# Kernel tuning notes

Hardware: AMD Instinct MI355X
Metric: run time of the kernel (lower is better)

Reference implementation:

```python
import jax, jax.numpy as jnp
from jax import lax
import numpy as np

B = 32          # batch
E = 768         # embedding_dim == hidden_dim (required for the module to run)
V = 8192        # vocabulary_size
MAX_LEN = 256   # max_seq_length


def setup_inputs() -> dict:
    key = jax.random.key(0)
    ks = jax.random.split(key, 10)
    s = 0.02
    return {
        "latent": jax.random.normal(ks[0], (B, E), jnp.float32),
        "W_lat": jax.random.normal(ks[1], (E, E), jnp.float32) * s,
        "b_lat": jnp.zeros((E,), jnp.float32),
        "emb":   jax.random.normal(ks[2], (V, E), jnp.float32) * s,
        "W_ih":  jax.random.normal(ks[3], (3 * E, E), jnp.float32) * s,
        "W_hh":  jax.random.normal(ks[4], (3 * E, E), jnp.float32) * s,
        "b_ih":  jnp.zeros((3 * E,), jnp.float32),
        "b_hh":  jnp.zeros((3 * E,), jnp.float32),
        "W_out": jax.random.normal(ks[5], (V, E), jnp.float32) * s,
        "b_out": jnp.zeros((V,), jnp.float32),
    }


def reference(latent, W_lat, b_lat, emb, W_ih, W_hh, b_ih, b_hh, W_out, b_out):
    # initial hidden state: projected latent, shape [B, E]
    h0 = latent @ W_lat.T + b_lat
    # decoder starts from token id 1 (<sos>)
    tok0 = jnp.ones((latent.shape[0],), jnp.int32)

    def step(carry, _):
        h, tok = carry
        x = emb[tok]                                  # [B, E] embedding lookup
        gi = x @ W_ih.T + b_ih                        # [B, 3E]
        gh = h @ W_hh.T + b_hh                        # [B, 3E]
        i_r, i_z, i_n = jnp.split(gi, 3, axis=-1)
        h_r, h_z, h_n = jnp.split(gh, 3, axis=-1)
        r = jax.nn.sigmoid(i_r + h_r)
        z = jax.nn.sigmoid(i_z + h_z)
        n = jnp.tanh(i_n + r * h_n)
        h_new = (1.0 - z) * n + z * h                 # torch GRU cell update
        pred = h_new @ W_out.T + b_out                # [B, V]
        tok_new = jnp.argmax(pred, axis=-1).astype(jnp.int32)  # greedy decode
        return (h_new, tok_new), pred

    _, preds = lax.scan(step, (h0, tok0), None, length=MAX_LEN)  # [T, B, V]
    return preds.transpose(1, 0, 2)                               # [B, T, V]
```

## Files before the change

### kernel.cpp

```cpp
#include <hip/hip_runtime.h>
#include <stdint.h>


typedef unsigned long long u64;
typedef unsigned int u32;
typedef _Float16 f16;
using half8 = __attribute__((ext_vector_type(8))) _Float16;
using f32x4 = __attribute__((ext_vector_type(4))) float;
using uint4v = __attribute__((ext_vector_type(4))) unsigned int;

#define E_ 768
#define V_ 8192
#define T_ 256
#define HP 24576
#define IH_PLANE (2304*768)
#define OUT_PLANE (8192*768)
#define NBLK 256

#define AGENT_LD(p)    __hip_atomic_load((p), __ATOMIC_RELAXED, __HIP_MEMORY_SCOPE_AGENT)
#define AGENT_ST(p,v)  __hip_atomic_store((p), (v), __ATOMIC_RELAXED, __HIP_MEMORY_SCOPE_AGENT)
#define AGENT_ADD(p,v) __hip_atomic_fetch_add((p), (v), __ATOMIC_RELAXED, __HIP_MEMORY_SCOPE_AGENT)

__device__ __forceinline__ f32x4 mfma16(half8 a, half8 b, f32x4 c){
  return __builtin_amdgcn_mfma_f32_16x16x32_f16(a, b, c, 0, 0, 0);
}
__device__ __forceinline__ void split2(float f, f16& hi, f16& lo){
  f16 h = (f16)f; hi = h; lo = (f16)((f - (float)h) * 4096.0f);
}
__device__ __forceinline__ u32 packh(float f){
  f16 h, l; split2(f, h, l);
  return (u32)__builtin_bit_cast(unsigned short, h) |
         ((u32)__builtin_bit_cast(unsigned short, l) << 16);
}
__device__ __forceinline__ float unpackh(u32 u){
  f16 h = __builtin_bit_cast(f16, (unsigned short)(u & 0xffffu));
  f16 l = __builtin_bit_cast(f16, (unsigned short)(u >> 16));
  return (float)h + (float)l * (1.0f/4096.0f);
}
__device__ __forceinline__ u64 packkey(float f, int v){
  u32 fb = __float_as_uint(f);
  u32 s  = fb ^ ((u32)((int32_t)fb>>31) | 0x80000000u);
  return ((u64)s<<32) | (u64)(0xFFFFFFFFu - (u32)v);
}

#define NB_CONV 1200
#define NB_H0   96
#define NG_IH   221184
#define NG_ALL  1228800

__global__ __launch_bounds__(256) void prep_k(
    const float* __restrict__ W_ih, const float* __restrict__ W_hh, const float* __restrict__ W_out,
    const float* __restrict__ latent, const float* __restrict__ W_lat, const float* __restrict__ b_lat,
    f16* __restrict__ Wih_s, f16* __restrict__ Whh_s, f16* __restrict__ Wout_s,
    float* __restrict__ h_f32, u32* __restrict__ h_seq, unsigned* __restrict__ bar)
{
  int blk = blockIdx.x;
  if (blk < NB_CONV){
    for (int g = blk*256 + threadIdx.x; g < NG_ALL; g += NB_CONV*256){
      const float* src; f16* hi; f16* lo; int off;
      if (g < NG_IH)        { src=W_ih; hi=Wih_s; lo=Wih_s+IH_PLANE; off=g*8; }
      else if (g < 2*NG_IH) { src=W_hh; hi=Whh_s; lo=Whh_s+IH_PLANE; off=(g-NG_IH)*8; }
      else                  { src=W_out; hi=Wout_s; lo=Wout_s+OUT_PLANE; off=(g-2*NG_IH)*8; }
      float4 a = *(const float4*)(src+off);
      float4 b = *(const float4*)(src+off+4);
      float fs[8] = {a.x,a.y,a.z,a.w,b.x,b.y,b.z,b.w};
      half8 vh, vl;
      #pragma unroll
      for (int j=0;j<8;j++){ f16 h,l; split2(fs[j],h,l); vh[j]=h; vl[j]=l; }
      *(half8*)(hi+off) = vh;
      *(half8*)(lo+off) = vl;
    }
  } else {
    if (blk==NB_CONV) bar[threadIdx.x] = 0;
    int tid = (blk-NB_CONV)*256 + threadIdx.x;
    int b = tid/768, e = tid - b*768;
    const float4* wr = (const float4*)(W_lat + (size_t)e*768);
    const float4* xr = (const float4*)(latent + (size_t)b*768);
    float s0=0.f,s1=0.f,s2=0.f,s3=0.f;
    for (int k=0;k<192;k++){
      float4 w = wr[k]; float4 x = xr[k];
      s0 += w.x*x.x; s1 += w.y*x.y; s2 += w.z*x.z; s3 += w.w*x.w;
    }
    float acc = b_lat[e] + ((s0+s1)+(s2+s3));
    h_f32[b*768+e] = acc;
    h_seq[b*768+e] = packh(acc);
  }
}

__global__ __launch_bounds__(512) void gitab_k(
    const float* __restrict__ emb, const f16* __restrict__ Wih_s, u32* __restrict__ gi_tab)
{
  __shared__ float red[3][8][2][64][4];
  const int bid = blockIdx.x, tid = threadIdx.x;
  const int tb = bid>>1, half = bid&1;
  const int w = tid>>6, lane = tid&63, col = lane&15, kg = lane>>4, kc = w;
  half8 ah[2][3], al[2][3];
  #pragma unroll
  for (int m=0;m<2;m++)
    #pragma unroll
    for (int i=0;i<3;i++){
      const float* src = emb + (size_t)(tb*32 + m*16 + col)*768 + kc*96 + i*32 + kg*8;
      float4 x0 = *(const float4*)src, x1 = *(const float4*)(src+4);
      float fs[8] = {x0.x,x0.y,x0.z,x0.w,x1.x,x1.y,x1.z,x1.w};
      half8 vh, vl;
      #pragma unroll
      for (int j=0;j<8;j++){ f16 h,l; split2(fs[j],h,l); vh[j]=h; vl[j]=l; }
      ah[m][i]=vh; al[m][i]=vl;
    }
  for (int g=0; g<24; ++g){
    #pragma unroll
    for (int j=0;j<3;j++){
      const int nt = half*72 + g*3 + j;
      f32x4 a0[2], a1[2];
      #pragma unroll
      for (int m=0;m<2;m++){ a0[m]=f32x4{0,0,0,0}; a1[m]=f32x4{0,0,0,0}; }
      #pragma unroll
      for (int i=0;i<3;i++){
        size_t o = (size_t)(nt*16+col)*768 + kc*96 + i*32 + kg*8;
        half8 bh = *(const half8*)(Wih_s + o);
        half8 bl = *(const half8*)(Wih_s + IH_PLANE + o);
        #pragma unroll
        for (int m=0;m<2;m++){
          a0[m] = mfma16(ah[m][i], bh, a0[m]);
          a1[m] = mfma16(ah[m][i], bl, a1[m]);
          a1[m] = mfma16(al[m][i], bh, a1[m]);
        }
      }
      #pragma unroll
      for (int m=0;m<2;m++){
        f32x4 v;
        #pragma unroll
        for (int r=0;r<4;r++) v[r] = a0[m][r] + a1[m][r]*(1.0f/4096.0f);
        *(f32x4*)&red[j][w][m][lane][0] = v;
      }
    }
    __syncthreads();
    if (w < 6){
      const int j = w>>1, m = w&1;
      f32x4 s = {0,0,0,0};
      #pragma unroll
      for (int ww=0; ww<8; ww++) s += *(const f32x4*)&red[j][ww][m][lane][0];
      const int nt = half*72 + g*3 + j;
      const int tokr = tb*32 + m*16 + kg*4;
      #pragma unroll
      for (int r=0;r<4;r++)
        gi_tab[(size_t)(tokr+r)*2304 + nt*16 + col] = packh(s[r]);
    }
    __syncthreads();
  }
}

__device__ __forceinline__ void gridbar(unsigned* bar, unsigned target){
  __syncthreads();
  if (threadIdx.x == 0){
    const int g = blockIdx.x & 7;
    unsigned old = AGENT_ADD(&bar[g*16], 1u);
    if (old == 32u*target - 1u)
      AGENT_ADD(&bar[128], 1u);
    int spins = 0;
    while (AGENT_LD(&bar[128]) < 8u*target){
      __builtin_amdgcn_s_sleep(1);
      if ((++spins & 2047) == 0)
        AGENT_ADD(&bar[128], 0u);
    }
  }
  __syncthreads();
}

__global__ __launch_bounds__(512, 2) void decode_k(
    const f16* __restrict__ Wout_s, const f16* __restrict__ Whh_s, const u32* __restrict__ gi_tab,
    float* __restrict__ gh_buf, const float* __restrict__ h_f32, u32* __restrict__ h_seq,
    u64* __restrict__ candbufT, const float* __restrict__ b_ih, const float* __restrict__ b_hh,
    const float* __restrict__ b_out, float* __restrict__ out, unsigned* __restrict__ bar)
{
  __shared__ float red[3][8][2][64][4];
  __shared__ u64 amkey[32];
  const int bid = blockIdx.x, tid = threadIdx.x;
  const int w = tid>>6, lane = tid&63, col = lane&15, kg = lane>>4, kc = w;

  __builtin_amdgcn_fence(__ATOMIC_ACQUIRE, "agent");
  __syncthreads();

  const f16* srcH[3] = {Wout_s, Wout_s, (bid<144)? Whh_s : Wout_s};
  const f16* srcL[3] = {Wout_s+OUT_PLANE, Wout_s+OUT_PLANE,
                        (bid<144)? Whh_s+IH_PLANE : Wout_s+OUT_PLANE};
  const int  rowb[3] = {bid*16, 4096+bid*16, (bid<144)? bid*16 : 0};
  half8 bf_h[3][3], bf_l[3][3];
  #pragma unroll
  for (int s=0;s<3;s++)
    #pragma unroll
    for (int i=0;i<3;i++){
      size_t o = (size_t)(rowb[s]+col)*768 + kc*96 + i*32 + kg*8;
      bf_h[s][i] = *(const half8*)(srcH[s] + o);
      bf_l[s][i] = *(const half8*)(srcL[s] + o);
    }
  float bo_reg[2];
  bo_reg[0] = b_out[bid*16 + col];
  bo_reg[1] = b_out[4096 + bid*16 + col];

  int cb = 0, ce = 0; float hreg = 0.f;
  float bir=0,biz=0,bin_=0,bhr=0,bhz=0,bhn=0;
  if (bid < 48){
    int gid = bid*512 + tid;
    cb = gid/768; ce = gid - cb*768;
    hreg = h_f32[cb*768 + ce];
    bir=b_ih[ce]; biz=b_ih[768+ce]; bin_=b_ih[1536+ce];
    bhr=b_hh[ce]; bhz=b_hh[768+ce]; bhn=b_hh[1536+ce];
  }

  unsigned bt = 0;
  for (int t=0; t<=256; ++t){
    if (tid < 32) amkey[tid] = 0;
    const u32* hbase = h_seq + (size_t)t*HP;
    uint4v qa[2][3], qb[2][3];
    #pragma unroll
    for (int m=0;m<2;m++)
      #pragma unroll
      for (int i=0;i<3;i++){
        const uint4v* hp = (const uint4v*)(hbase + (m*16+col)*768 + kc*96 + i*32 + kg*8);
        qa[m][i] = hp[0];
        qb[m][i] = hp[1];
      }
    half8 ah[2][3], al[2][3];
    #pragma unroll
    for (int m=0;m<2;m++)
      #pragma unroll
      for (int i=0;i<3;i++){
        uint4v wh, wl;
        u32 d[8] = {qa[m][i][0],qa[m][i][1],qa[m][i][2],qa[m][i][3],
                    qb[m][i][0],qb[m][i][1],qb[m][i][2],qb[m][i][3]};
        #pragma unroll
        for (int j=0;j<4;j++){
          u32 w0 = d[2*j], w1 = d[2*j+1];
          wh[j] = (w0 & 0xffffu) | (w1 << 16);
          wl[j] = (w0 >> 16) | (w1 & 0xffff0000u);
        }
        ah[m][i] = __builtin_bit_cast(half8, wh);
        al[m][i] = __builtin_bit_cast(half8, wl);
      }
    #pragma unroll
    for (int s=0;s<3;s++){
      f32x4 a0[2], a1[2];
      #pragma unroll
      for (int m=0;m<2;m++){ a0[m]=f32x4{0,0,0,0}; a1[m]=f32x4{0,0,0,0}; }
      #pragma unroll
      for (int i=0;i<3;i++)
        #pragma unroll
        for (int m=0;m<2;m++){
          a0[m] = mfma16(ah[m][i], bf_h[s][i], a0[m]);
          a1[m] = mfma16(ah[m][i], bf_l[s][i], a1[m]);
          a1[m] = mfma16(al[m][i], bf_h[s][i], a1[m]);
        }
      #pragma unroll
      for (int m=0;m<2;m++){
        f32x4 v;
        #pragma unroll
        for (int r=0;r<4;r++) v[r] = a0[m][r] + a1[m][r]*(1.0f/4096.0f);
        *(f32x4*)&red[s][w][m][lane][0] = v;
      }
    }
    __syncthreads();
    float sv[2][4];
    bool have_out = false;
    if (w < 3){
      const int s = w;
      float vm[2][4];
      #pragma unroll
      for (int m=0;m<2;m++){
        f32x4 sum = {0,0,0,0};
        #pragma unroll
        for (int ww=0; ww<8; ww++) sum += *(const f32x4*)&red[s][ww][m][lane][0];
        #pragma unroll
        for (int r=0;r<4;r++) vm[m][r] = sum[r];
      }
      if (s < 2){
        if (t >= 1){
          have_out = true;
          const int v = s*4096 + bid*16 + col;
          const float bo = bo_reg[s];
          #pragma unroll
          for (int m=0;m<2;m++)
            #pragma unroll
            for (int r=0;r<4;r++){
              const int b = m*16 + kg*4 + r;
              const float p = vm[m][r] + bo;
              sv[m][r] = p;
              u64 key = packkey(p, v);
              #pragma unroll
              for (int off=1; off<16; off<<=1){
                u64 o = __shfl_xor((unsigned long long)key, off);
                if (o > key) key = o;
              }
              if (col == 0) atomicMax(&amkey[b], key);
            }
        }
      } else if (bid < 144){
        const int gr = bid*16 + col;
        #pragma unroll
        for (int m=0;m<2;m++)
          #pragma unroll
          for (int r=0;r<4;r++)
            AGENT_ST(&gh_buf[(m*16+kg*4+r)*2304 + gr], vm[m][r]);
      }
    }
    __syncthreads();
    if (t >= 1 && tid < 32) AGENT_ST(&candbufT[(size_t)tid*256 + bid], amkey[tid]);
    if (t == 256){
      if (have_out){
        const int v = w*4096 + bid*16 + col;
        #pragma unroll
        for (int m=0;m<2;m++)
          #pragma unroll
          for (int r=0;r<4;r++)
            out[(size_t)(m*16+kg*4+r)*((size_t)T_*V_) + (size_t)(t-1)*V_ + v] = sv[m][r];
      }
      break;
    }
    gridbar(bar, ++bt);
    if (bid >= 48){
      if (have_out){
        const int v = w*4096 + bid*16 + col;
        #pragma unroll
        for (int m=0;m<2;m++)
          #pragma unroll
          for (int r=0;r<4;r++)
            out[(size_t)(m*16+kg*4+r)*((size_t)T_*V_) + (size_t)(t-1)*V_ + v] = sv[m][r];
      }
    } else {
      int tok = 1;
      if (t > 0){
        u64 k = 0;
        #pragma unroll
        for (int j=0;j<4;j++){
          u64 c = AGENT_LD(&candbufT[(size_t)cb*256 + lane + 64*j]);
          if (c > k) k = c;
        }
        #pragma unroll
        for (int off=1; off<64; off<<=1){
          u64 o = __shfl_xor((unsigned long long)k, off);
          if (o > k) k = o;
        }
        tok = (int)(0xFFFFFFFFu - (unsigned)(k & 0xFFFFFFFFull));
      }
      const u32* gp = gi_tab + (size_t)tok*2304 + ce;
      const float gir = unpackh(gp[0])    + bir;
      const float giz = unpackh(gp[768])  + biz;
      const float gin = unpackh(gp[1536]) + bin_;
      float* hb = gh_buf + cb*2304 + ce;
      const float ghr = AGENT_LD(hb)        + bhr;
      const float ghz = AGENT_LD(hb + 768)  + bhz;
      const float ghn = AGENT_LD(hb + 1536) + bhn;
      const float rr = 1.0f/(1.0f+expf(-(gir+ghr)));
      const float zz = 1.0f/(1.0f+expf(-(giz+ghz)));
      const float nn = tanhf(gin + rr*ghn);
      hreg = (1.0f-zz)*nn + zz*hreg;
      AGENT_ST(&h_seq[(size_t)(t+1)*HP + cb*768 + ce], packh(hreg));
      if (have_out){
        const int v = w*4096 + bid*16 + col;
        #pragma unroll
        for (int m=0;m<2;m++)
          #pragma unroll
          for (int r=0;r<4;r++)
            out[(size_t)(m*16+kg*4+r)*((size_t)T_*V_) + (size_t)(t-1)*V_ + v] = sv[m][r];
      }
    }
    gridbar(bar, ++bt);
  }
}

extern "C" void kernel_launch(void* const* d_in, const int* in_sizes, int n_in,
                              void* d_out, int out_size, void* d_ws, size_t ws_size,
                              hipStream_t stream){
  const float* latent = (const float*)d_in[0];
  const float* W_lat  = (const float*)d_in[1];
  const float* b_lat  = (const float*)d_in[2];
  const float* emb    = (const float*)d_in[3];
  const float* W_ih   = (const float*)d_in[4];
  const float* W_hh   = (const float*)d_in[5];
  const float* b_ih   = (const float*)d_in[6];
  const float* b_hh   = (const float*)d_in[7];
  const float* W_out  = (const float*)d_in[8];
  const float* b_out  = (const float*)d_in[9];
  float* out = (float*)d_out;
  (void)in_sizes; (void)n_in; (void)out_size; (void)ws_size;

  char* ws = (char*)d_ws;
  size_t off = 0;
  auto carve = [&](size_t bytes)->char*{
    char* p = ws + off; off += (bytes + 255) & ~(size_t)255; return p;
  };
  f16*      Wih_s  = (f16*)     carve((size_t)2*IH_PLANE*2);
  f16*      Whh_s  = (f16*)     carve((size_t)2*IH_PLANE*2);
  f16*      Wout_s = (f16*)     carve((size_t)2*OUT_PLANE*2);
  u32*      gi_tab = (u32*)     carve((size_t)8192*2304*4);
  float*    gh_buf = (float*)   carve((size_t)32*2304*4);
  float*    h_f32  = (float*)   carve((size_t)HP*4);
  u32*      h_seq  = (u32*)     carve((size_t)257*HP*4);
  u64*      candbufT=(u64*)     carve((size_t)32*256*8);
  unsigned* bar    = (unsigned*)carve(2048);

  hipLaunchKernelGGL(prep_k, dim3(NB_CONV+NB_H0), dim3(256), 0, stream,
                     W_ih, W_hh, W_out, latent, W_lat, b_lat,
                     Wih_s, Whh_s, Wout_s, h_f32, h_seq, bar);
  hipLaunchKernelGGL(gitab_k, dim3(512), dim3(512), 0, stream, emb, Wih_s, gi_tab);

  void* kargs[] = {
    (void*)&Wout_s, (void*)&Whh_s, (void*)&gi_tab, (void*)&gh_buf, (void*)&h_f32,
    (void*)&h_seq, (void*)&candbufT, (void*)&b_ih, (void*)&b_hh, (void*)&b_out,
    (void*)&out, (void*)&bar
  };
  (void)hipLaunchCooperativeKernel((void*)decode_k, dim3(NBLK), dim3(512), kargs, 0, stream);
}
```

Baseline: 3.083 ms.

## Pre-split hidden-state layout, flat grid barrier, interleaved gh buffer, earlier output stores

Stores the hidden state as separate hi/lo f16 halves in MFMA-ready 8-element groups, so the per-step A-operand load becomes direct half8 reads with no repacking. The grid barrier becomes a single level of 16 counters polled by one wavefront with __all, replacing the two-level counter scheme. gh_buf is interleaved per (batch, element) so the three gate values sit next to each other, and they are loaded earlier together with the logit stores. The h_seq writes use inline-asm short stores with sc0 sc1 plus a vmcnt wait, which depends on hardware-specific cache semantics for visibility to other blocks.

```diff
diff --git a/kernel.cpp b/kernel.cpp
--- a/kernel.cpp
+++ b/kernel.cpp
@@ -4,10 +4,10 @@
 
 typedef unsigned long long u64;
 typedef unsigned int u32;
+typedef unsigned short ush;
 typedef _Float16 f16;
 using half8 = __attribute__((ext_vector_type(8))) _Float16;
 using f32x4 = __attribute__((ext_vector_type(4))) float;
-using uint4v = __attribute__((ext_vector_type(4))) unsigned int;
 
 #define E_ 768
 #define V_ 8192
@@ -16,6 +16,8 @@
 #define IH_PLANE (2304*768)
 #define OUT_PLANE (8192*768)
 #define NBLK 256
+#define HS_STEP 49152
+#define HS_ROW  1536
 
 #define AGENT_LD(p)    __hip_atomic_load((p), __ATOMIC_RELAXED, __HIP_MEMORY_SCOPE_AGENT)
 #define AGENT_ST(p,v)  __hip_atomic_store((p), (v), __ATOMIC_RELAXED, __HIP_MEMORY_SCOPE_AGENT)
@@ -29,12 +31,11 @@
 }
 __device__ __forceinline__ u32 packh(float f){
   f16 h, l; split2(f, h, l);
-  return (u32)__builtin_bit_cast(unsigned short, h) |
-         ((u32)__builtin_bit_cast(unsigned short, l) << 16);
+  return (u32)__builtin_bit_cast(ush, h) | ((u32)__builtin_bit_cast(ush, l) << 16);
 }
 __device__ __forceinline__ float unpackh(u32 u){
-  f16 h = __builtin_bit_cast(f16, (unsigned short)(u & 0xffffu));
-  f16 l = __builtin_bit_cast(f16, (unsigned short)(u >> 16));
+  f16 h = __builtin_bit_cast(f16, (ush)(u & 0xffffu));
+  f16 l = __builtin_bit_cast(f16, (ush)(u >> 16));
   return (float)h + (float)l * (1.0f/4096.0f);
 }
 __device__ __forceinline__ u64 packkey(float f, int v){
@@ -83,7 +84,10 @@
     }
     float acc = b_lat[e] + ((s0+s1)+(s2+s3));
     h_f32[b*768+e] = acc;
-    h_seq[b*768+e] = packh(acc);
+    f16 hh, ll; split2(acc, hh, ll);
+    ush* hw = (ush*)h_seq + b*HS_ROW + (e>>3)*16 + (e&7);
+    hw[0] = __builtin_bit_cast(ush, hh);
+    hw[8] = __builtin_bit_cast(ush, ll);
   }
 }
 
@@ -152,16 +156,14 @@
 
 __device__ __forceinline__ void gridbar(unsigned* bar, unsigned target){
   __syncthreads();
-  if (threadIdx.x == 0){
-    const int g = blockIdx.x & 7;
-    unsigned old = AGENT_ADD(&bar[g*16], 1u);
-    if (old == 32u*target - 1u)
-      AGENT_ADD(&bar[128], 1u);
-    int spins = 0;
-    while (AGENT_LD(&bar[128]) < 8u*target){
+  if (threadIdx.x < 64){
+    if (threadIdx.x == 0) AGENT_ADD(&bar[(blockIdx.x & 15)*16], 1u);
+    const u32 goal = 16u*target;
+    const int lane = threadIdx.x;
+    for(;;){
+      u32 v = (lane < 16) ? AGENT_LD(&bar[lane*16]) : goal;
+      if (__all(v >= goal)) break;
       __builtin_amdgcn_s_sleep(1);
-      if ((++spins & 2047) == 0)
-        AGENT_ADD(&bar[128], 0u);
     }
   }
   __syncthreads();
@@ -207,36 +209,21 @@
     bir=b_ih[ce]; biz=b_ih[768+ce]; bin_=b_ih[1536+ce];
     bhr=b_hh[ce]; bhz=b_hh[768+ce]; bhn=b_hh[1536+ce];
   }
+  const int gr2 = bid*16 + col;
+  const int gg2 = gr2/768, ge2 = gr2 - (gr2/768)*768;
 
   unsigned bt = 0;
   for (int t=0; t<=256; ++t){
     if (tid < 32) amkey[tid] = 0;
-    const u32* hbase = h_seq + (size_t)t*HP;
-    uint4v qa[2][3], qb[2][3];
-    #pragma unroll
-    for (int m=0;m<2;m++)
-      #pragma unroll
-      for (int i=0;i<3;i++){
-        const uint4v* hp = (const uint4v*)(hbase + (m*16+col)*768 + kc*96 + i*32 + kg*8);
-        qa[m][i] = hp[0];
-        qb[m][i] = hp[1];
-      }
+    const ush* h16 = (const ush*)h_seq + (size_t)t*HS_STEP;
     half8 ah[2][3], al[2][3];
     #pragma unroll
     for (int m=0;m<2;m++)
       #pragma unroll
       for (int i=0;i<3;i++){
-        uint4v wh, wl;
-        u32 d[8] = {qa[m][i][0],qa[m][i][1],qa[m][i][2],qa[m][i][3],
-                    qb[m][i][0],qb[m][i][1],qb[m][i][2],qb[m][i][3]};
-        #pragma unroll
-        for (int j=0;j<4;j++){
-          u32 w0 = d[2*j], w1 = d[2*j+1];
-          wh[j] = (w0 & 0xffffu) | (w1 << 16);
-          wl[j] = (w0 >> 16) | (w1 & 0xffff0000u);
-        }
-        ah[m][i] = __builtin_bit_cast(half8, wh);
-        al[m][i] = __builtin_bit_cast(half8, wl);
+        const ush* hp = h16 + (m*16+col)*HS_ROW + (kc*12+i*4+kg)*16;
+        ah[m][i] = *(const half8*)(hp);
+        al[m][i] = *(const half8*)(hp+8);
       }
     #pragma unroll
     for (int s=0;s<3;s++){
@@ -295,12 +282,11 @@
             }
         }
       } else if (bid < 144){
-        const int gr = bid*16 + col;
         #pragma unroll
         for (int m=0;m<2;m++)
           #pragma unroll
           for (int r=0;r<4;r++)
-            AGENT_ST(&gh_buf[(m*16+kg*4+r)*2304 + gr], vm[m][r]);
+            AGENT_ST(&gh_buf[((size_t)(m*16+kg*4+r)*768 + ge2)*4 + gg2], vm[m][r]);
       }
     }
     __syncthreads();
@@ -327,6 +313,18 @@
             out[(size_t)(m*16+kg*4+r)*((size_t)T_*V_) + (size_t)(t-1)*V_ + v] = sv[m][r];
       }
     } else {
+      const float* hb4 = gh_buf + ((size_t)cb*768 + ce)*4;
+      const float ghr0 = AGENT_LD(hb4 + 0);
+      const float ghz0 = AGENT_LD(hb4 + 1);
+      const float ghn0 = AGENT_LD(hb4 + 2);
+      if (have_out){
+        const int v = w*4096 + bid*16 + col;
+        #pragma unroll
+        for (int m=0;m<2;m++)
+          #pragma unroll
+          for (int r=0;r<4;r++)
+            out[(size_t)(m*16+kg*4+r)*((size_t)T_*V_) + (size_t)(t-1)*V_ + v] = sv[m][r];
+      }
       int tok = 1;
       if (t > 0){
         u64 k = 0;
@@ -346,23 +344,20 @@
       const float gir = unpackh(gp[0])    + bir;
       const float giz = unpackh(gp[768])  + biz;
       const float gin = unpackh(gp[1536]) + bin_;
-      float* hb = gh_buf + cb*2304 + ce;
-      const float ghr = AGENT_LD(hb)        + bhr;
-      const float ghz = AGENT_LD(hb + 768)  + bhz;
-      const float ghn = AGENT_LD(hb + 1536) + bhn;
+      const float ghr = ghr0 + bhr;
+      const float ghz = ghz0 + bhz;
+      const float ghn = ghn0 + bhn;
       const float rr = 1.0f/(1.0f+expf(-(gir+ghr)));
       const float zz = 1.0f/(1.0f+expf(-(giz+ghz)));
       const float nn = tanhf(gin + rr*ghn);
       hreg = (1.0f-zz)*nn + zz*hreg;
-      AGENT_ST(&h_seq[(size_t)(t+1)*HP + cb*768 + ce], packh(hreg));
-      if (have_out){
-        const int v = w*4096 + bid*16 + col;
-        #pragma unroll
-        for (int m=0;m<2;m++)
-          #pragma unroll
-          for (int r=0;r<4;r++)
-            out[(size_t)(m*16+kg*4+r)*((size_t)T_*V_) + (size_t)(t-1)*V_ + v] = sv[m][r];
-      }
+      f16 hh, ll; split2(hreg, hh, ll);
+      ush* hw = (ush*)h_seq + (size_t)(t+1)*HS_STEP + cb*HS_ROW + (ce>>3)*16 + (ce&7);
+      u32 hbits = (u32)__builtin_bit_cast(ush, hh);
+      u32 lbits = (u32)__builtin_bit_cast(ush, ll);
+      asm volatile("global_store_short %0, %1, off sc0 sc1" :: "v"(hw),   "v"(hbits) : "memory");
+      asm volatile("global_store_short %0, %1, off sc0 sc1" :: "v"(hw+8), "v"(lbits) : "memory");
+      asm volatile("s_waitcnt vmcnt(0)" ::: "memory");
     }
     gridbar(bar, ++bt);
   }
@@ -393,7 +388,7 @@
   f16*      Whh_s  = (f16*)     carve((size_t)2*IH_PLANE*2);
   f16*      Wout_s = (f16*)     carve((size_t)2*OUT_PLANE*2);
   u32*      gi_tab = (u32*)     carve((size_t)8192*2304*4);
-  float*    gh_buf = (float*)   carve((size_t)32*2304*4);
+  float*    gh_buf = (float*)   carve((size_t)32*768*4*4);
   float*    h_f32  = (float*)   carve((size_t)HP*4);
   u32*      h_seq  = (u32*)     carve((size_t)257*HP*4);
   u64*      candbufT=(u64*)     carve((size_t)32*256*8);
```

Result: slower. 3.360 ms (+9.0%).
